# Optimization experiments

Hardware: AMD Instinct MI355X
Metric: run time of the kernel (lower is better)

## Reference

```python
import jax, jax.numpy as jnp
import numpy as np
from jax import lax

HEADS = 8
DIM_HEAD = 8
SCALE = DIM_HEAD ** (-0.5)
UP = 64  # nn.Upsample(scale_factor=64), nearest


def _conv_s8(x, w, b):
    # Conv2d(inner, inner, 11x11, stride 8, padding 2) + exact GELU
    y = lax.conv_general_dilated(x, w, window_strides=(8, 8),
                                 padding=((2, 2), (2, 2)),
                                 dimension_numbers=('NCHW', 'OIHW', 'NCHW'))
    return jax.nn.gelu(y + b[None, :, None, None], approximate=False)


def setup_inputs() -> dict:
    key = jax.random.key(0)
    ks = jax.random.split(key, 8)
    b, c, h, w = 2, 64, 48, 48
    inner = HEADS * DIM_HEAD  # 64
    f = jax.random.normal(ks[0], (b, c, h, w), jnp.float32)
    w_qkv = jax.random.normal(ks[1], (inner * 3, c, 1, 1), jnp.float32) * 0.05
    wq = jax.random.normal(ks[2], (inner, inner, 11, 11), jnp.float32) * 0.02
    bq = jax.random.normal(ks[3], (inner,), jnp.float32) * 0.02
    wk = jax.random.normal(ks[4], (inner, inner, 11, 11), jnp.float32) * 0.02
    bk = jax.random.normal(ks[5], (inner,), jnp.float32) * 0.02
    pos_h = jax.random.normal(ks[6], (DIM_HEAD, h), jnp.float32) * SCALE
    pos_w = jax.random.normal(ks[7], (DIM_HEAD, w), jnp.float32) * SCALE
    return {"f": f, "w_qkv": w_qkv, "wq": wq, "bq": bq, "wk": wk,
            "bk": bk, "pos_h": pos_h, "pos_w": pos_w}


def reference(f, w_qkv, wq, bq, wk, bk, pos_h, pos_w):
    b, c, h, w = f.shape
    inner = HEADS * DIM_HEAD
    # 1x1 conv to qkv
    qkv = jnp.einsum('oc,bchw->bohw', w_qkv[:, :, 0, 0], f)
    q, k, v = jnp.split(qkv, 3, axis=1)  # each [b, inner, h, w]
    # positional logits from pre-conv q
    q_full = q.reshape(b, HEADS, DIM_HEAD, h * w)
    emb = (pos_h[:, :, None] + pos_w[:, None, :]).reshape(DIM_HEAD, h * w)
    pos_logits = jnp.einsum('bhci,cj->bhij', q_full, emb)  # [b,H,hw,hw]
    # strided conv + gelu on q,k
    qd = _conv_s8(q, wq, bq)
    kd = _conv_s8(k, wk, bk)
    m = qd.shape[-1]  # downsampled side
    qd = qd.reshape(b, HEADS, DIM_HEAD, m * m) * SCALE
    kd = kd.reshape(b, HEADS, DIM_HEAD, m * m)
    vv = v.reshape(b, HEADS, DIM_HEAD, h * w)
    dots = jnp.einsum('bhci,bhcj->bhij', qd, kd)  # [b,H,m^2,m^2]
    # nearest upsample x64 on last two dims
    dots = jnp.repeat(jnp.repeat(dots, UP, axis=-2), UP, axis=-1)
    attn = jax.nn.softmax(dots + pos_logits, axis=-1)
    fmap = jnp.einsum('bhij,bhcj->bhci', attn, vv)
    return fmap.reshape(b, inner, h, w)
```

## Files before the change

kernel.cpp:

```cpp
#include <hip/hip_runtime.h>
#include <math.h>

#define HW 2304
#define O192 192
#define SCALE_F 0.35355339059327373f

typedef unsigned int u32;
typedef __attribute__((address_space(1))) const u32 gu32;
typedef __attribute__((address_space(3))) u32 lu32;
__device__ __forceinline__ void dma16(const void* g, void* l) {
  __builtin_amdgcn_global_load_lds((gu32*)g, (lu32*)l, 16, 0, 0);
}

__global__ __launch_bounds__(256) void qkv_kernel(
    const float* __restrict__ F, const float* __restrict__ W,
    float* __restrict__ QKV, float* __restrict__ V2) {
  __shared__ __align__(16) float sW[384];
  int blk = blockIdx.x;
  int idx0 = blk * 256;
  int r0 = idx0 / HW;
  int r1 = (idx0 + 255) / HW;
  int tid = threadIdx.x;
  if (tid < 192) {
    int g = tid >> 6, c = tid & 63;
    sW[tid]       = W[((r0 & 63) + g * 64) * 64 + c];
    sW[192 + tid] = W[((r1 & 63) + g * 64) * 64 + c];
  }
  __syncthreads();
  int idx = idx0 + tid;
  int p  = idx % HW;
  int r  = idx / HW;
  int o0 = r & 63;
  int b  = r >> 6;
  const float4* w4 = (const float4*)(sW + ((r == r0) ? 0 : 192));
  const float* f = F + (b * 64) * HW + p;
  float aq = 0.f, ak = 0.f, av = 0.f;
  #pragma unroll 4
  for (int c4 = 0; c4 < 16; c4++) {
    float4 wq = w4[c4];
    float4 wk = w4[16 + c4];
    float4 wv = w4[32 + c4];
    float f0 = f[(c4 * 4 + 0) * HW];
    float f1 = f[(c4 * 4 + 1) * HW];
    float f2 = f[(c4 * 4 + 2) * HW];
    float f3 = f[(c4 * 4 + 3) * HW];
    aq = fmaf(wq.x, f0, aq); ak = fmaf(wk.x, f0, ak); av = fmaf(wv.x, f0, av);
    aq = fmaf(wq.y, f1, aq); ak = fmaf(wk.y, f1, ak); av = fmaf(wv.y, f1, av);
    aq = fmaf(wq.z, f2, aq); ak = fmaf(wk.z, f2, ak); av = fmaf(wv.z, f2, av);
    aq = fmaf(wq.w, f3, aq); ak = fmaf(wk.w, f3, ak); av = fmaf(wv.w, f3, av);
  }
  float* qp = QKV + (b * HW + p) * O192;
  qp[o0]      = aq;
  qp[o0 + 64] = ak;
  V2[(((b << 3) + (o0 >> 3)) * HW + p) * 8 + (o0 & 7)] = av;
}

__global__ __launch_bounds__(256) void conv_kernel(
    const float* __restrict__ QKV, const float* __restrict__ Wq,
    const float* __restrict__ Bq, const float* __restrict__ Wk,
    const float* __restrict__ Bk, float* __restrict__ QD) {
  __shared__ float sW[7744];
  __shared__ float sRed[4 * 64 * 6];
  int blk = blockIdx.x;
  int xcd = blk & 7;
  int T = xcd >> 2, b = (xcd >> 1) & 1, s = xcd & 1;
  int idx = (blk >> 3) * 2 + s;
  int o  = idx / 6;
  int oy = idx % 6;
  const float* Wg = T ? Wk : Wq;
  for (int i = threadIdx.x; i < 7744; i += 256) sW[i] = Wg[o * 7744 + i];
  __syncthreads();
  int wv = threadIdx.x >> 6;
  int c  = threadIdx.x & 63;
  const float* base = QKV + b * (HW * O192) + T * 64 + c;
  float acc[6];
  #pragma unroll
  for (int ox = 0; ox < 6; ox++) acc[ox] = 0.f;
  for (int kyi = 0; kyi < 3; kyi++) {
    int ky = wv * 3 + kyi;
    if (ky > 10) break;
    int y = oy * 8 - 2 + ky;
    if ((unsigned)y < 48u) {
      float xrow[48];
      #pragma unroll
      for (int x = 0; x < 48; x++) xrow[x] = base[(y * 48 + x) * O192];
      #pragma unroll
      for (int kx = 0; kx < 11; kx++) {
        float wt = sW[c * 121 + ky * 11 + kx];
        #pragma unroll
        for (int ox = 0; ox < 6; ox++) {
          int x = ox * 8 - 2 + kx;
          if (x >= 0 && x < 48) acc[ox] = fmaf(xrow[x], wt, acc[ox]);
        }
      }
    }
  }
  #pragma unroll
  for (int ox = 0; ox < 6; ox++) sRed[(wv * 64 + c) * 6 + ox] = acc[ox];
  __syncthreads();
  if (threadIdx.x < 64) {
    int t = threadIdx.x;
    float r[6];
    #pragma unroll
    for (int ox = 0; ox < 6; ox++)
      r[ox] = sRed[t * 6 + ox] + sRed[(64 + t) * 6 + ox]
            + sRed[(128 + t) * 6 + ox] + sRed[(192 + t) * 6 + ox];
    #pragma unroll
    for (int off = 32; off; off >>= 1) {
      #pragma unroll
      for (int ox = 0; ox < 6; ox++) r[ox] += __shfl_down(r[ox], off, 64);
    }
    if (t == 0) {
      float bias = T ? Bk[o] : Bq[o];
      #pragma unroll
      for (int ox = 0; ox < 6; ox++) {
        float g = r[ox] + bias;
        float ge = 0.5f * g * (1.0f + erff(g * 0.70710678118654752f));
        QD[((T * 2 + b) * 64 + o) * 36 + oy * 6 + ox] = ge;
      }
    }
  }
}

#define OFF_V   0
#define OFF_EA  4608
#define OFF_PHT 4992
#define OFF_PWT 5376
#define OFF_E   5760
#define OFF_QT  5800
#define OFF_R   6056
#define SBUF_N  7208

__global__ __launch_bounds__(256) void attn_kernel(
    const float* __restrict__ QKV, const float* __restrict__ V2,
    const float* __restrict__ QD, const float* __restrict__ PH,
    const float* __restrict__ PW, float* __restrict__ out) {
  __shared__ __align__(16) float sB[SBUF_N];
  int blk = blockIdx.x;
  int bh = blk / 72;
  int S  = blk - bh * 72;
  int b = bh >> 3, h = bh & 7;
  int tid = threadIdx.x;
  int w = tid >> 6, lane = tid & 63;
  int rl16 = lane & 15;
  int g  = w * 4 + (lane >> 4);
  for (int t = tid; t < 384; t += 256) {
    sB[OFF_PHT + t] = PH[(t & 7) * 48 + (t >> 3)];
    sB[OFF_PWT + t] = PW[(t & 7) * 48 + (t >> 3)];
  }
  if (tid < 36) {
    int I = S >> 1;
    float acc = 0.f;
    #pragma unroll
    for (int c8 = 0; c8 < 8; c8++) {
      float qv = QD[((0 + b) * 64 + h * 8 + c8) * 36 + I];
      float kv = QD[((2 + b) * 64 + h * 8 + c8) * 36 + tid];
      acc = fmaf(qv, kv, acc);
    }
    sB[OFF_E + tid] = __expf(SCALE_F * acc);
  }
  {
    int row = tid >> 3, c = tid & 7;
    sB[OFF_QT + c * 32 + row] =
      QKV[(b * HW + S * 32 + row) * O192 + h * 8 + c];
  }
  {
    const char* src = (const char*)(V2 + (size_t)bh * (HW * 8));
    for (int m = w; m < 18; m += 4)
      dma16(src + m * 1024 + lane * 16, (char*)(sB + OFF_V) + m * 1024);
  }
  __syncthreads();
  float eB[2][3];
  #pragma unroll
  for (int k = 0; k < 2; k++) {
    int row = rl16 + k * 16;
    #pragma unroll
    for (int i = 0; i < 3; i++) {
      const float* pp = sB + OFF_PWT + (g * 3 + i) * 8;
      float d = 0.f;
      #pragma unroll
      for (int j = 0; j < 8; j++) d = fmaf(sB[OFF_QT + j * 32 + row], pp[j], d);
      eB[k][i] = __expf(d);
    }
  }
  float acc0[9], acc1[9];
  #pragma unroll
  for (int c = 0; c < 9; c++) { acc0[c] = 0.f; acc1[c] = 0.f; }
  const float4* sV4 = (const float4*)(sB + OFF_V);
  #pragma unroll 1
  for (int q = 0; q < 4; q++) {
    for (int t = tid; t < 384; t += 256) {
      int jyL = t >> 5, rr = t & 31;
      const float* pp = sB + OFF_PHT + (q * 12 + jyL) * 8;
      float d = 0.f;
      #pragma unroll
      for (int j = 0; j < 8; j++) d = fmaf(sB[OFF_QT + j * 32 + rr], pp[j], d);
      sB[OFF_EA + jyL * 32 + ((rr & 15) << 1) + (rr >> 4)] = __expf(d);
    }
    __syncthreads();
    #pragma unroll 1
    for (int jyL = 0; jyL < 12; jyL++) {
      float2 eA = *(const float2*)(sB + OFF_EA + jyL * 32 + rl16 * 2);
      int cb = (q * 12 + jyL) * 48 + g * 3;
      int J0 = cb >> 6, J1 = (cb + 2) >> 6;
      int ib = 64 - (cb & 63);
      float e0 = sB[OFF_E + J0];
      float e1 = sB[OFF_E + J1];
      float a00 = eA.x * e0, a01 = eA.x * e1;
      float a10 = eA.y * e0, a11 = eA.y * e1;
      #pragma unroll
      for (int i = 0; i < 3; i++) {
        float4 vlo = sV4[(jyL * 48 + g * 3 + i) * 2];
        float4 vhi = sV4[(jyL * 48 + g * 3 + i) * 2 + 1];
        bool sel = (i < ib);
        float w0 = (sel ? a00 : a01) * eB[0][i];
        float w1 = (sel ? a10 : a11) * eB[1][i];
        acc0[0] = fmaf(w0, vlo.x, acc0[0]);  acc1[0] = fmaf(w1, vlo.x, acc1[0]);
        acc0[1] = fmaf(w0, vlo.y, acc0[1]);  acc1[1] = fmaf(w1, vlo.y, acc1[1]);
        acc0[2] = fmaf(w0, vlo.z, acc0[2]);  acc1[2] = fmaf(w1, vlo.z, acc1[2]);
        acc0[3] = fmaf(w0, vlo.w, acc0[3]);  acc1[3] = fmaf(w1, vlo.w, acc1[3]);
        acc0[4] = fmaf(w0, vhi.x, acc0[4]);  acc1[4] = fmaf(w1, vhi.x, acc1[4]);
        acc0[5] = fmaf(w0, vhi.y, acc0[5]);  acc1[5] = fmaf(w1, vhi.y, acc1[5]);
        acc0[6] = fmaf(w0, vhi.z, acc0[6]);  acc1[6] = fmaf(w1, vhi.z, acc1[6]);
        acc0[7] = fmaf(w0, vhi.w, acc0[7]);  acc1[7] = fmaf(w1, vhi.w, acc1[7]);
        acc0[8] += w0;                        acc1[8] += w1;
      }
    }
    if (q < 3) {
      __syncthreads();
      const char* src = (const char*)(V2 + (size_t)bh * (HW * 8) + (size_t)(q + 1) * 4608);
      for (int m = w; m < 18; m += 4)
        dma16(src + m * 1024 + lane * 16, (char*)(sB + OFF_V) + m * 1024);
    }
  }
  #pragma unroll
  for (int c = 0; c < 9; c++) {
    acc0[c] += __shfl_xor(acc0[c], 16, 64);
    acc0[c] += __shfl_xor(acc0[c], 32, 64);
    acc1[c] += __shfl_xor(acc1[c], 16, 64);
    acc1[c] += __shfl_xor(acc1[c], 32, 64);
  }
  if ((lane & 48) == 0) {
    #pragma unroll
    for (int c = 0; c < 9; c++) {
      sB[OFF_R + ((w * 2 + 0) * 16 + rl16) * 9 + c] = acc0[c];
      sB[OFF_R + ((w * 2 + 1) * 16 + rl16) * 9 + c] = acc1[c];
    }
  }
  __syncthreads();
  {
    int c = tid >> 5, r = tid & 31;
    int k = r >> 4, r16 = r & 15;
    float num = 0.f, z = 0.f;
    #pragma unroll
    for (int ww = 0; ww < 4; ww++) {
      num += sB[OFF_R + ((ww * 2 + k) * 16 + r16) * 9 + c];
      z   += sB[OFF_R + ((ww * 2 + k) * 16 + r16) * 9 + 8];
    }
    out[(b * 64 + h * 8 + c) * HW + S * 32 + r] = num / z;
  }
}

extern "C" void kernel_launch(void* const* d_in, const int* in_sizes, int n_in,
                              void* d_out, int out_size, void* d_ws, size_t ws_size,
                              hipStream_t stream) {
  const float* F    = (const float*)d_in[0];
  const float* Wqkv = (const float*)d_in[1];
  const float* Wq   = (const float*)d_in[2];
  const float* Bq   = (const float*)d_in[3];
  const float* Wk   = (const float*)d_in[4];
  const float* Bk   = (const float*)d_in[5];
  const float* PH   = (const float*)d_in[6];
  const float* PW   = (const float*)d_in[7];
  float* out = (float*)d_out;

  float* ws   = (float*)d_ws;
  float* QKV  = ws;
  float* V2   = QKV + 2 * HW * O192;
  float* QD   = V2 + 2 * 8 * HW * 8;

  qkv_kernel <<<1152, 256, 0, stream>>>(F, Wqkv, QKV, V2);
  conv_kernel<<<1536, 256, 0, stream>>>(QKV, Wq, Bq, Wk, Bk, QD);
  attn_kernel<<<1152, 256, 0, stream>>>(QKV, V2, QD, PH, PW, out);
}
```

Before: 133.2 us.

## Prefetch next V chunk into registers and double-buffer exp tables

The attention kernel now loads the next V chunk from global memory into registers at the start of each iteration and writes it to LDS after the compute loop, replacing the direct global-to-LDS DMA issued after compute. The per-chunk exp(row logits) table is double-buffered and computed one chunk ahead, which removes a barrier before each compute phase. The aim is to hide global load latency behind the FMA loop. The cost is extra registers (five float4 per thread), which could hurt occupancy, plus a larger LDS footprint.

```diff
diff --git a/kernel.cpp b/kernel.cpp
--- a/kernel.cpp
+++ b/kernel.cpp
@@ -124,12 +124,12 @@
 
 #define OFF_V   0
 #define OFF_EA  4608
-#define OFF_PHT 4992
-#define OFF_PWT 5376
-#define OFF_E   5760
-#define OFF_QT  5800
-#define OFF_R   6056
-#define SBUF_N  7208
+#define OFF_PHT 5376
+#define OFF_PWT 5760
+#define OFF_E   6144
+#define OFF_QT  6184
+#define OFF_R   6440
+#define SBUF_N  7592
 
 __global__ __launch_bounds__(256) void attn_kernel(
     const float* __restrict__ QKV, const float* __restrict__ V2,
@@ -183,24 +183,44 @@
       eB[k][i] = __expf(d);
     }
   }
+  for (int t = tid; t < 384; t += 256) {
+    int jyL = t >> 5, rr = t & 31;
+    const float* pp = sB + OFF_PHT + jyL * 8;
+    float d = 0.f;
+    #pragma unroll
+    for (int j = 0; j < 8; j++) d = fmaf(sB[OFF_QT + j * 32 + rr], pp[j], d);
+    sB[OFF_EA + jyL * 32 + ((rr & 15) << 1) + (rr >> 4)] = __expf(d);
+  }
+  __syncthreads();
   float acc0[9], acc1[9];
   #pragma unroll
   for (int c = 0; c < 9; c++) { acc0[c] = 0.f; acc1[c] = 0.f; }
   const float4* sV4 = (const float4*)(sB + OFF_V);
+  const float4* vsrc4 = (const float4*)(V2 + (size_t)bh * (HW * 8));
   #pragma unroll 1
   for (int q = 0; q < 4; q++) {
-    for (int t = tid; t < 384; t += 256) {
-      int jyL = t >> 5, rr = t & 31;
-      const float* pp = sB + OFF_PHT + (q * 12 + jyL) * 8;
-      float d = 0.f;
-      #pragma unroll
-      for (int j = 0; j < 8; j++) d = fmaf(sB[OFF_QT + j * 32 + rr], pp[j], d);
-      sB[OFF_EA + jyL * 32 + ((rr & 15) << 1) + (rr >> 4)] = __expf(d);
-    }
-    __syncthreads();
+    float4 pf0, pf1, pf2, pf3, pf4;
+    if (q < 3) {
+      const float4* src = vsrc4 + (q + 1) * 1152;
+      pf0 = src[tid];
+      pf1 = src[tid + 256];
+      pf2 = src[tid + 512];
+      pf3 = src[tid + 768];
+      if (tid < 128) pf4 = src[tid + 1024];
+      int eaN = ((q + 1) & 1) * 384;
+      for (int t = tid; t < 384; t += 256) {
+        int jyL = t >> 5, rr = t & 31;
+        const float* pp = sB + OFF_PHT + ((q + 1) * 12 + jyL) * 8;
+        float d = 0.f;
+        #pragma unroll
+        for (int j = 0; j < 8; j++) d = fmaf(sB[OFF_QT + j * 32 + rr], pp[j], d);
+        sB[OFF_EA + eaN + jyL * 32 + ((rr & 15) << 1) + (rr >> 4)] = __expf(d);
+      }
+    }
+    const float* eAb = sB + OFF_EA + (q & 1) * 384;
     #pragma unroll 1
     for (int jyL = 0; jyL < 12; jyL++) {
-      float2 eA = *(const float2*)(sB + OFF_EA + jyL * 32 + rl16 * 2);
+      float2 eA = *(const float2*)(eAb + jyL * 32 + rl16 * 2);
       int cb = (q * 12 + jyL) * 48 + g * 3;
       int J0 = cb >> 6, J1 = (cb + 2) >> 6;
       int ib = 64 - (cb & 63);
@@ -228,9 +248,13 @@
     }
     if (q < 3) {
       __syncthreads();
-      const char* src = (const char*)(V2 + (size_t)bh * (HW * 8) + (size_t)(q + 1) * 4608);
-      for (int m = w; m < 18; m += 4)
-        dma16(src + m * 1024 + lane * 16, (char*)(sB + OFF_V) + m * 1024);
+      float4* vdst4 = (float4*)(sB + OFF_V);
+      vdst4[tid]       = pf0;
+      vdst4[tid + 256] = pf1;
+      vdst4[tid + 512] = pf2;
+      vdst4[tid + 768] = pf3;
+      if (tid < 128) vdst4[tid + 1024] = pf4;
+      __syncthreads();
     }
   }
   #pragma unroll
```

Result: no change. 133.4 us (+0.2%).

## Fold 1x1 qkv weights into strided conv weights and merge front kernels

Applied to the files above, without the earlier changes.

Precomposes the 1x1 qkv projection with the 11x11 strided conv weights, so the conv reads F directly instead of waiting for the QKV output. This removes the dependency between the two front stages and lets them run as one launch: 128 blocks do the fused conv and the rest compute QKV/V. The cost is that each conv block now loops serially over both batches and all 6 output rows, so a few long-running blocks could dominate the front launch.

```diff
diff --git a/kernel.cpp b/kernel.cpp
--- a/kernel.cpp
+++ b/kernel.cpp
@@ -12,113 +12,125 @@
   __builtin_amdgcn_global_load_lds((gu32*)g, (lu32*)l, 16, 0, 0);
 }
 
-__global__ __launch_bounds__(256) void qkv_kernel(
-    const float* __restrict__ F, const float* __restrict__ W,
-    float* __restrict__ QKV, float* __restrict__ V2) {
-  __shared__ __align__(16) float sW[384];
+__global__ __launch_bounds__(256) void front_kernel(
+    const float* __restrict__ F, const float* __restrict__ Wqkv,
+    const float* __restrict__ Wq, const float* __restrict__ Bq,
+    const float* __restrict__ Wk, const float* __restrict__ Bk,
+    float* __restrict__ QKV, float* __restrict__ V2, float* __restrict__ QD) {
+  __shared__ __align__(16) float sS[9792];
   int blk = blockIdx.x;
-  int idx0 = blk * 256;
-  int r0 = idx0 / HW;
-  int r1 = (idx0 + 255) / HW;
   int tid = threadIdx.x;
-  if (tid < 192) {
-    int g = tid >> 6, c = tid & 63;
-    sW[tid]       = W[((r0 & 63) + g * 64) * 64 + c];
-    sW[192 + tid] = W[((r1 & 63) + g * 64) * 64 + c];
-  }
-  __syncthreads();
-  int idx = idx0 + tid;
-  int p  = idx % HW;
-  int r  = idx / HW;
-  int o0 = r & 63;
-  int b  = r >> 6;
-  const float4* w4 = (const float4*)(sW + ((r == r0) ? 0 : 192));
-  const float* f = F + (b * 64) * HW + p;
-  float aq = 0.f, ak = 0.f, av = 0.f;
-  #pragma unroll 4
-  for (int c4 = 0; c4 < 16; c4++) {
-    float4 wq = w4[c4];
-    float4 wk = w4[16 + c4];
-    float4 wv = w4[32 + c4];
-    float f0 = f[(c4 * 4 + 0) * HW];
-    float f1 = f[(c4 * 4 + 1) * HW];
-    float f2 = f[(c4 * 4 + 2) * HW];
-    float f3 = f[(c4 * 4 + 3) * HW];
-    aq = fmaf(wq.x, f0, aq); ak = fmaf(wk.x, f0, ak); av = fmaf(wv.x, f0, av);
-    aq = fmaf(wq.y, f1, aq); ak = fmaf(wk.y, f1, ak); av = fmaf(wv.y, f1, av);
-    aq = fmaf(wq.z, f2, aq); ak = fmaf(wk.z, f2, ak); av = fmaf(wv.z, f2, av);
-    aq = fmaf(wq.w, f3, aq); ak = fmaf(wk.w, f3, ak); av = fmaf(wv.w, f3, av);
-  }
-  float* qp = QKV + (b * HW + p) * O192;
-  qp[o0]      = aq;
-  qp[o0 + 64] = ak;
-  V2[(((b << 3) + (o0 >> 3)) * HW + p) * 8 + (o0 & 7)] = av;
-}
-
-__global__ __launch_bounds__(256) void conv_kernel(
-    const float* __restrict__ QKV, const float* __restrict__ Wq,
-    const float* __restrict__ Bq, const float* __restrict__ Wk,
-    const float* __restrict__ Bk, float* __restrict__ QD) {
-  __shared__ float sW[7744];
-  __shared__ float sRed[4 * 64 * 6];
-  int blk = blockIdx.x;
-  int xcd = blk & 7;
-  int T = xcd >> 2, b = (xcd >> 1) & 1, s = xcd & 1;
-  int idx = (blk >> 3) * 2 + s;
-  int o  = idx / 6;
-  int oy = idx % 6;
-  const float* Wg = T ? Wk : Wq;
-  for (int i = threadIdx.x; i < 7744; i += 256) sW[i] = Wg[o * 7744 + i];
-  __syncthreads();
-  int wv = threadIdx.x >> 6;
-  int c  = threadIdx.x & 63;
-  const float* base = QKV + b * (HW * O192) + T * 64 + c;
-  float acc[6];
-  #pragma unroll
-  for (int ox = 0; ox < 6; ox++) acc[ox] = 0.f;
-  for (int kyi = 0; kyi < 3; kyi++) {
-    int ky = wv * 3 + kyi;
-    if (ky > 10) break;
-    int y = oy * 8 - 2 + ky;
-    if ((unsigned)y < 48u) {
-      float xrow[48];
-      #pragma unroll
-      for (int x = 0; x < 48; x++) xrow[x] = base[(y * 48 + x) * O192];
-      #pragma unroll
-      for (int kx = 0; kx < 11; kx++) {
-        float wt = sW[c * 121 + ky * 11 + kx];
+  if (blk < 128) {
+    int T = blk >> 6, o = blk & 63;
+    const float* Wg = (T ? Wk : Wq) + o * 7744;
+    float* sWq = sS;
+    float* sWe = sS + 2048;
+    for (int half = 0; half < 2; half++) {
+      for (int i = tid; i < 2048; i += 256)
+        sWq[i] = Wqkv[(T * 64 + half * 32 + (i >> 6)) * 64 + (i & 63)];
+      __syncthreads();
+      for (int j = tid; j < 7744; j += 256) {
+        int cp = j / 121, t1 = j - cp * 121;
+        float s = (half == 0) ? 0.f : sWe[j];
         #pragma unroll
-        for (int ox = 0; ox < 6; ox++) {
-          int x = ox * 8 - 2 + kx;
-          if (x >= 0 && x < 48) acc[ox] = fmaf(xrow[x], wt, acc[ox]);
+        for (int ci = 0; ci < 32; ci++)
+          s = fmaf(Wg[(half * 32 + ci) * 121 + t1], sWq[ci * 64 + cp], s);
+        sWe[j] = s;
+      }
+      __syncthreads();
+    }
+    int wv = tid >> 6, c = tid & 63;
+    float bias = T ? Bk[o] : Bq[o];
+    float* sRed = sS;
+    for (int bi = 0; bi < 2; bi++) {
+      const float* base = F + (bi * 64 + c) * HW;
+      for (int oy = 0; oy < 6; oy++) {
+        float acc[6];
+        #pragma unroll
+        for (int ox = 0; ox < 6; ox++) acc[ox] = 0.f;
+        for (int kyi = 0; kyi < 3; kyi++) {
+          int ky = wv * 3 + kyi;
+          if (ky > 10) break;
+          int y = oy * 8 - 2 + ky;
+          if ((unsigned)y < 48u) {
+            float xrow[48];
+            #pragma unroll
+            for (int x = 0; x < 48; x++) xrow[x] = base[y * 48 + x];
+            #pragma unroll
+            for (int kx = 0; kx < 11; kx++) {
+              float wt = sWe[c * 121 + ky * 11 + kx];
+              #pragma unroll
+              for (int ox = 0; ox < 6; ox++) {
+                int x = ox * 8 - 2 + kx;
+                if (x >= 0 && x < 48) acc[ox] = fmaf(xrow[x], wt, acc[ox]);
+              }
+            }
+          }
+        }
+        __syncthreads();
+        #pragma unroll
+        for (int ox = 0; ox < 6; ox++) sRed[(wv * 64 + c) * 6 + ox] = acc[ox];
+        __syncthreads();
+        if (tid < 64) {
+          float r[6];
+          #pragma unroll
+          for (int ox = 0; ox < 6; ox++)
+            r[ox] = sRed[tid * 6 + ox] + sRed[(64 + tid) * 6 + ox]
+                  + sRed[(128 + tid) * 6 + ox] + sRed[(192 + tid) * 6 + ox];
+          #pragma unroll
+          for (int off = 32; off; off >>= 1) {
+            #pragma unroll
+            for (int ox = 0; ox < 6; ox++) r[ox] += __shfl_down(r[ox], off, 64);
+          }
+          if (tid == 0) {
+            #pragma unroll
+            for (int ox = 0; ox < 6; ox++) {
+              float g = r[ox] + bias;
+              QD[((T * 2 + bi) * 64 + o) * 36 + oy * 6 + ox] =
+                0.5f * g * (1.0f + erff(g * 0.70710678118654752f));
+            }
+          }
         }
       }
     }
-  }
-  #pragma unroll
-  for (int ox = 0; ox < 6; ox++) sRed[(wv * 64 + c) * 6 + ox] = acc[ox];
-  __syncthreads();
-  if (threadIdx.x < 64) {
-    int t = threadIdx.x;
-    float r[6];
-    #pragma unroll
-    for (int ox = 0; ox < 6; ox++)
-      r[ox] = sRed[t * 6 + ox] + sRed[(64 + t) * 6 + ox]
-            + sRed[(128 + t) * 6 + ox] + sRed[(192 + t) * 6 + ox];
-    #pragma unroll
-    for (int off = 32; off; off >>= 1) {
-      #pragma unroll
-      for (int ox = 0; ox < 6; ox++) r[ox] += __shfl_down(r[ox], off, 64);
-    }
-    if (t == 0) {
-      float bias = T ? Bk[o] : Bq[o];
-      #pragma unroll
-      for (int ox = 0; ox < 6; ox++) {
-        float g = r[ox] + bias;
-        float ge = 0.5f * g * (1.0f + erff(g * 0.70710678118654752f));
-        QD[((T * 2 + b) * 64 + o) * 36 + oy * 6 + ox] = ge;
-      }
-    }
+  } else {
+    int qb = blk - 128;
+    float* sW = sS;
+    int idx0 = qb * 256;
+    int r0 = idx0 / HW;
+    int r1 = (idx0 + 255) / HW;
+    if (tid < 192) {
+      int g = tid >> 6, c = tid & 63;
+      sW[tid]       = Wqkv[((r0 & 63) + g * 64) * 64 + c];
+      sW[192 + tid] = Wqkv[((r1 & 63) + g * 64) * 64 + c];
+    }
+    __syncthreads();
+    int idx = idx0 + tid;
+    int p  = idx % HW;
+    int r  = idx / HW;
+    int o0 = r & 63;
+    int b  = r >> 6;
+    const float4* w4 = (const float4*)(sW + ((r == r0) ? 0 : 192));
+    const float* f = F + (b * 64) * HW + p;
+    float aq = 0.f, ak = 0.f, av = 0.f;
+    #pragma unroll 4
+    for (int c4 = 0; c4 < 16; c4++) {
+      float4 wq = w4[c4];
+      float4 wk = w4[16 + c4];
+      float4 wv = w4[32 + c4];
+      float f0 = f[(c4 * 4 + 0) * HW];
+      float f1 = f[(c4 * 4 + 1) * HW];
+      float f2 = f[(c4 * 4 + 2) * HW];
+      float f3 = f[(c4 * 4 + 3) * HW];
+      aq = fmaf(wq.x, f0, aq); ak = fmaf(wk.x, f0, ak); av = fmaf(wv.x, f0, av);
+      aq = fmaf(wq.y, f1, aq); ak = fmaf(wk.y, f1, ak); av = fmaf(wv.y, f1, av);
+      aq = fmaf(wq.z, f2, aq); ak = fmaf(wk.z, f2, ak); av = fmaf(wv.z, f2, av);
+      aq = fmaf(wq.w, f3, aq); ak = fmaf(wk.w, f3, ak); av = fmaf(wv.w, f3, av);
+    }
+    float* qp = QKV + (b * HW + p) * O192;
+    qp[o0]      = aq;
+    qp[o0 + 64] = ak;
+    V2[(((b << 3) + (o0 >> 3)) * HW + p) * 8 + (o0 & 7)] = av;
   }
 }
 
@@ -279,7 +291,6 @@
   float* V2   = QKV + 2 * HW * O192;
   float* QD   = V2 + 2 * 8 * HW * 8;
 
-  qkv_kernel <<<1152, 256, 0, stream>>>(F, Wqkv, QKV, V2);
-  conv_kernel<<<1536, 256, 0, stream>>>(QKV, Wq, Bq, Wk, Bk, QD);
-  attn_kernel<<<1152, 256, 0, stream>>>(QKV, V2, QD, PH, PW, out);
-}
+  front_kernel<<<1280, 256, 0, stream>>>(F, Wqkv, Wq, Bq, Wk, Bk, QKV, V2, QD);
+  attn_kernel <<<1152, 256, 0, stream>>>(QKV, V2, QD, PH, PW, out);
+}
```

New measurement: 180.8 us. 1.36x slower.
